# Performance work log

Measured on AMD Instinct MI355X. Metric: run time of the kernel, lower is better.

Reference implementation:

```python
import jax, jax.numpy as jnp
import numpy as np

B, S, DIM = 8, 1, 2048
H = 16
QLR, KVLR = 1536, 512
DN, DR, DV = 128, 64, 128      # qk_nope, qk_rope, v head dims
START = 8191                    # start_pos; end_pos = START + S = 8192
EPS = 1e-6
SCALE = (DN + DR) ** -0.5


def _rms(x, w):
    # F.rms_norm: x / sqrt(mean(x^2)+eps) * w
    return x * w * jax.lax.rsqrt(jnp.mean(jnp.square(x), axis=-1, keepdims=True) + EPS)


def _rope(x, cos, sin):
    # x: [..., r]; consecutive pairs (x0,x1) treated as complex, multiplied by cos+i*sin
    xr, xi = x[..., 0::2], x[..., 1::2]
    out_r = xr * cos - xi * sin
    out_i = xr * sin + xi * cos
    return jnp.stack([out_r, out_i], axis=-1).reshape(x.shape)


def setup_inputs() -> dict:
    key = jax.random.key(0)
    ks = jax.random.split(key, 12)
    # rotary tables for the single decode position
    inv_freq = 1.0 / (10000.0 ** (np.arange(0, DR, 2, dtype=np.float32) / DR))  # [DR/2]
    pos = np.arange(START, START + S, dtype=np.float32)[:, None]                # [S,1]
    ang = pos * inv_freq[None, :]                                               # [S, DR/2]
    return {
        "x": jax.random.normal(ks[0], (B, S, DIM), jnp.float32),
        "start_pos": START,
        "freqs_cos": jnp.asarray(np.cos(ang)),
        "freqs_sin": jnp.asarray(np.sin(ang)),
        "kv_cache_prefix": jax.random.normal(ks[1], (B, START, KVLR), jnp.float32),
        "pe_cache_prefix": jax.random.normal(ks[2], (B, START, DR), jnp.float32),
        "wq_a_w": jax.random.normal(ks[3], (QLR, DIM), jnp.float32) * 0.02,
        "wq_a_b": jnp.zeros((QLR,), jnp.float32),
        "q_norm_w": jnp.ones((QLR,), jnp.float32),
        "wq_b_w": jax.random.normal(ks[4], (H * (DN + DR), QLR), jnp.float32) * 0.02,
        "wq_b_b": jnp.zeros((H * (DN + DR),), jnp.float32),
        "wkv_a_w": jax.random.normal(ks[5], (KVLR + DR, DIM), jnp.float32) * 0.02,
        "wkv_a_b": jnp.zeros((KVLR + DR,), jnp.float32),
        "kv_norm_w": jnp.ones((KVLR,), jnp.float32),
        "wkv_b_w": jax.random.normal(ks[6], (H * (DN + DV), KVLR), jnp.float32) * 0.02,
        "wo_w": jax.random.normal(ks[7], (DIM, H * DV), jnp.float32) * 0.02,
        "wo_b": jnp.zeros((DIM,), jnp.float32),
    }


def reference(x, start_pos, freqs_cos, freqs_sin, kv_cache_prefix, pe_cache_prefix,
              wq_a_w, wq_a_b, q_norm_w, wq_b_w, wq_b_b,
              wkv_a_w, wkv_a_b, kv_norm_w, wkv_b_w, wo_w, wo_b):
    b, s, _ = x.shape
    # low-rank query projection
    q = _rms(x @ wq_a_w.T + wq_a_b, q_norm_w) @ wq_b_w.T + wq_b_b
    q = q.reshape(b, s, H, DN + DR)
    q_nope, q_pe = q[..., :DN], q[..., DN:]
    cos = freqs_cos[None, :, None, :]  # [1,s,1,DR/2]
    sin = freqs_sin[None, :, None, :]
    q_pe = _rope(q_pe, cos, sin)
    # compressed KV + rope key branch
    kvpe = x @ wkv_a_w.T + wkv_a_b               # [b,s,KVLR+DR]
    kv, k_pe = kvpe[..., :KVLR], kvpe[..., KVLR:]
    k_pe = _rope(k_pe[:, :, None, :], cos, sin)[:, :, 0, :]
    # weight absorption: project q_nope into latent space through wkv_b's K-part
    wkv_b = wkv_b_w.reshape(H, DN + DV, KVLR)
    q_abs = jnp.einsum('bshd,hdc->bshc', q_nope, wkv_b[:, :DN])
    # append current step to caches
    kv_cache = jnp.concatenate([kv_cache_prefix, _rms(kv, kv_norm_w)], axis=1)  # [b,t,KVLR]
    pe_cache = jnp.concatenate([pe_cache_prefix, k_pe], axis=1)                 # [b,t,DR]
    # attention in latent space (seqlen=1 decode -> no causal mask needed)
    scores = (jnp.einsum('bshc,btc->bsht', q_abs, kv_cache)
              + jnp.einsum('bshr,btr->bsht', q_pe, pe_cache)) * SCALE
    attn = jax.nn.softmax(scores.astype(jnp.float32), axis=-1).astype(x.dtype)
    out = jnp.einsum('bsht,btc->bshc', attn, kv_cache)
    out = jnp.einsum('bshc,hdc->bshd', out, wkv_b[:, DN:])  # V-part of wkv_b
    return out.reshape(b, s, H * DV) @ wo_w.T + wo_b
```

## Files before the change

kernel.cpp:

```cpp
#include <hip/hip_runtime.h>
#include <math.h>

namespace {
constexpr int B_   = 8;
constexpr int DIM_ = 2048;
constexpr int H_   = 16;
constexpr int QLR_ = 1536;
constexpr int KVLR_= 512;
constexpr int DN_  = 128;
constexpr int DR_  = 64;
constexpr int DV_  = 128;
constexpr int TPRE_= 8191;
constexpr int CE_  = 576;
constexpr int NCH_ = 64;
constexpr int CT_  = 128;
constexpr int TS_  = 16;
constexpr int NS_  = CT_ / TS_;
constexpr int PSTR_= 20;
constexpr float EPS_ = 1e-6f;
constexpr float SCALE_ = 0.07216878364870322f;

constexpr size_t WS_QLAT  = 0;
constexpr size_t WS_KVPE  = WS_QLAT  + (size_t)B_*QLR_;
constexpr size_t WS_PENEW = WS_KVPE  + (size_t)B_*CE_;
constexpr size_t WS_QNOPE = WS_PENEW + (size_t)B_*DR_;
constexpr size_t WS_QT    = WS_QNOPE + (size_t)B_*H_*DN_;
constexpr size_t WS_MLOC  = WS_QT    + (size_t)B_*CE_*H_;
constexpr size_t WS_LLOC  = WS_MLOC  + (size_t)B_*H_*NCH_;
constexpr size_t WS_OUT2  = WS_LLOC  + (size_t)B_*H_*NCH_;
constexpr size_t WS_OPART = WS_OUT2  + (size_t)B_*DIM_;
}

__device__ __forceinline__ void gload16(const float* src, float* ldsDst) {
  __builtin_amdgcn_global_load_lds((const __attribute__((address_space(1))) void*)src,
                                   (__attribute__((address_space(3))) void*)ldsDst,
                                   16, 0, 0);
}

__device__ __forceinline__ float rsum16(float v) {
  int x = __float_as_int(v);
  v += __int_as_float(__builtin_amdgcn_update_dpp(0, x, 0xB1, 0xF, 0xF, true));
  x = __float_as_int(v);
  v += __int_as_float(__builtin_amdgcn_update_dpp(0, x, 0x4E, 0xF, 0xF, true));
  x = __float_as_int(v);
  v += __int_as_float(__builtin_amdgcn_update_dpp(0, x, 0x141, 0xF, 0xF, true));
  x = __float_as_int(v);
  v += __int_as_float(__builtin_amdgcn_update_dpp(0, x, 0x140, 0xF, 0xF, true));
  return v;
}

__device__ __forceinline__ void barrier_lgkm() {
  asm volatile("s_waitcnt lgkmcnt(0)" ::: "memory");
  __builtin_amdgcn_s_barrier();
  __builtin_amdgcn_sched_barrier(0);
}

__global__ __launch_bounds__(256) void mla_k1(const float* __restrict__ x,
                                              const float* __restrict__ wqa,
                                              const float* __restrict__ bqa,
                                              const float* __restrict__ wkva,
                                              const float* __restrict__ bkva,
                                              const float* __restrict__ fcos,
                                              const float* __restrict__ fsin,
                                              float* __restrict__ ws) {
  const int w = threadIdx.x >> 6, l = threadIdx.x & 63;
  const int r0 = (blockIdx.x * 4 + w) * 2;
  const float* W; const float* bias; int rr;
  if (r0 < QLR_) { W = wqa;  bias = bqa;  rr = r0; }
  else           { W = wkva; bias = bkva; rr = r0 - QLR_; }
  const float4* w0p = (const float4*)(W + (size_t)rr * DIM_);
  const float4* w1p = (const float4*)(W + (size_t)(rr + 1) * DIM_);
  const float4* x4  = (const float4*)x;
  float4 wv0[8], wv1[8];
#pragma unroll
  for (int j = 0; j < 8; ++j) { wv0[j] = w0p[l + 64 * j]; wv1[j] = w1p[l + 64 * j]; }
  float acc0[B_], acc1[B_];
#pragma unroll
  for (int b = 0; b < B_; ++b) { acc0[b] = 0.f; acc1[b] = 0.f; }
#pragma unroll
  for (int b = 0; b < B_; ++b) {
#pragma unroll
    for (int j = 0; j < 8; ++j) {
      const float4 xv = x4[b * (DIM_ / 4) + l + 64 * j];
      acc0[b] = fmaf(wv0[j].x, xv.x, fmaf(wv0[j].y, xv.y, fmaf(wv0[j].z, xv.z, fmaf(wv0[j].w, xv.w, acc0[b]))));
      acc1[b] = fmaf(wv1[j].x, xv.x, fmaf(wv1[j].y, xv.y, fmaf(wv1[j].z, xv.z, fmaf(wv1[j].w, xv.w, acc1[b]))));
    }
  }
#pragma unroll
  for (int b = 0; b < B_; ++b)
#pragma unroll
    for (int s = 32; s; s >>= 1) {
      acc0[b] += __shfl_xor(acc0[b], s);
      acc1[b] += __shfl_xor(acc1[b], s);
    }
  if (l == 0) {
    const float b0 = bias[rr], b1 = bias[rr + 1];
    if (r0 < QLR_) {
      float* out = ws + WS_QLAT;
#pragma unroll
      for (int b = 0; b < B_; ++b) {
        out[b * QLR_ + r0]     = acc0[b] + b0;
        out[b * QLR_ + r0 + 1] = acc1[b] + b1;
      }
    } else if (rr < KVLR_) {
      float* out = ws + WS_KVPE;
#pragma unroll
      for (int b = 0; b < B_; ++b) {
        out[b * CE_ + rr]     = acc0[b] + b0;
        out[b * CE_ + rr + 1] = acc1[b] + b1;
      }
    } else {
      const int i = (rr - KVLR_) >> 1;
      const float c = fcos[i], s = fsin[i];
      float* pen = ws + WS_PENEW;
#pragma unroll
      for (int b = 0; b < B_; ++b) {
        const float xr = acc0[b] + b0, xi = acc1[b] + b1;
        pen[b * DR_ + 2 * i]     = xr * c - xi * s;
        pen[b * DR_ + 2 * i + 1] = xr * s + xi * c;
      }
    }
  }
}

__global__ __launch_bounds__(256) void mla_k3(const float* __restrict__ qnw,
                                              const float* __restrict__ wqb,
                                              const float* __restrict__ bqb,
                                              const float* __restrict__ fcos,
                                              const float* __restrict__ fsin,
                                              float* __restrict__ ws) {
  __shared__ float qs_s[B_];
  const int tid = threadIdx.x;
  {
    const int bq = tid >> 5, l32 = tid & 31;
    const float4* ql4 = (const float4*)(ws + WS_QLAT + (size_t)bq * QLR_);
    float ss = 0.f;
#pragma unroll
    for (int j = 0; j < 12; ++j) {
      const float4 v = ql4[l32 + 32 * j];
      ss = fmaf(v.x, v.x, fmaf(v.y, v.y, fmaf(v.z, v.z, fmaf(v.w, v.w, ss))));
    }
#pragma unroll
    for (int d = 16; d; d >>= 1) ss += __shfl_xor(ss, d, 32);
    if (l32 == 0) qs_s[bq] = 1.0f / sqrtf(ss / (float)QLR_ + EPS_);
    __syncthreads();
  }
  const int w = tid >> 6, l = tid & 63;
  const int r0 = blockIdx.x * 8 + w * 2;
  const float4* w0p = (const float4*)(wqb + (size_t)r0 * QLR_);
  const float4* w1p = (const float4*)(wqb + (size_t)(r0 + 1) * QLR_);
  const float4* g4  = (const float4*)qnw;
  const float4* x4  = (const float4*)(ws + WS_QLAT);
  float4 wg0[6], wg1[6];
#pragma unroll
  for (int j = 0; j < 6; ++j) {
    const int c4 = l + 64 * j;
    const float4 a = w0p[c4], bb = w1p[c4], g = g4[c4];
    wg0[j].x = a.x * g.x; wg0[j].y = a.y * g.y; wg0[j].z = a.z * g.z; wg0[j].w = a.w * g.w;
    wg1[j].x = bb.x * g.x; wg1[j].y = bb.y * g.y; wg1[j].z = bb.z * g.z; wg1[j].w = bb.w * g.w;
  }
  float acc0[B_], acc1[B_];
#pragma unroll
  for (int b = 0; b < B_; ++b) { acc0[b] = 0.f; acc1[b] = 0.f; }
#pragma unroll
  for (int b = 0; b < B_; ++b) {
#pragma unroll
    for (int j = 0; j < 6; ++j) {
      const float4 xv = x4[b * (QLR_ / 4) + l + 64 * j];
      acc0[b] = fmaf(wg0[j].x, xv.x, fmaf(wg0[j].y, xv.y, fmaf(wg0[j].z, xv.z, fmaf(wg0[j].w, xv.w, acc0[b]))));
      acc1[b] = fmaf(wg1[j].x, xv.x, fmaf(wg1[j].y, xv.y, fmaf(wg1[j].z, xv.z, fmaf(wg1[j].w, xv.w, acc1[b]))));
    }
  }
#pragma unroll
  for (int b = 0; b < B_; ++b)
#pragma unroll
    for (int s = 32; s; s >>= 1) {
      acc0[b] += __shfl_xor(acc0[b], s);
      acc1[b] += __shfl_xor(acc1[b], s);
    }
  if (l == 0) {
    const int h = r0 / (DN_ + DR_);
    const int j0 = r0 - h * (DN_ + DR_);
    const float b0 = bqb[r0], b1 = bqb[r0 + 1];
    if (j0 < DN_) {
      float* qn = ws + WS_QNOPE;
#pragma unroll
      for (int b = 0; b < B_; ++b) {
        const float sb = qs_s[b];
        qn[(b * H_ + h) * DN_ + j0]     = acc0[b] * sb + b0;
        qn[(b * H_ + h) * DN_ + j0 + 1] = acc1[b] * sb + b1;
      }
    } else {
      const int i = (j0 - DN_) >> 1;
      const float c = fcos[i], s = fsin[i];
      float* qTT = ws + WS_QT;
#pragma unroll
      for (int b = 0; b < B_; ++b) {
        const float sb = qs_s[b];
        const float xr = acc0[b] * sb + b0, xi = acc1[b] * sb + b1;
        qTT[((size_t)(b * H_ + h)) * CE_ + KVLR_ + 2 * i]     = xr * c - xi * s;
        qTT[((size_t)(b * H_ + h)) * CE_ + KVLR_ + 2 * i + 1] = xr * s + xi * c;
      }
    }
  }
}

__global__ __launch_bounds__(256) void mla_k4(const float* __restrict__ wkvb,
                                              float* __restrict__ ws) {
  __shared__ float red[7 * 32 * B_];
  const int h = blockIdx.y;
  const int strip = blockIdx.x;
  const int tid = threadIdx.x;
  const int c = tid & 31, dg = tid >> 5;
  const int cg = strip * 32 + c;
  const float* qn = ws + WS_QNOPE;
  float acc[B_];
#pragma unroll
  for (int b = 0; b < B_; ++b) acc[b] = 0.f;
  const float* wp = wkvb + (size_t)h * 256 * KVLR_ + cg;
#pragma unroll
  for (int dd = 0; dd < 16; ++dd) {
    const int d = dg * 16 + dd;
    const float wv = wp[(size_t)d * KVLR_];
#pragma unroll
    for (int b = 0; b < B_; ++b) acc[b] = fmaf(qn[(b * H_ + h) * DN_ + d], wv, acc[b]);
  }
  if (dg > 0) {
#pragma unroll
    for (int b = 0; b < B_; ++b) red[(((dg - 1) * 32) + c) * B_ + b] = acc[b];
  }
  __syncthreads();
  if (dg == 0) {
    float* qTT = ws + WS_QT;
#pragma unroll
    for (int b = 0; b < B_; ++b) {
      float v = acc[b];
#pragma unroll
      for (int g = 0; g < 7; ++g) v += red[(g * 32 + c) * B_ + b];
      qTT[((size_t)(b * H_ + h)) * CE_ + cg] = v;
    }
  }
}

__global__ __launch_bounds__(512) void mla_k5(const float* __restrict__ kvpre,
                                              const float* __restrict__ pepre,
                                              const float* __restrict__ kvnw,
                                              float* __restrict__ ws) {
  __shared__ float kv_lds[2][TS_ * CE_];
  __shared__ float p_lds[TS_ * PSTR_];
  __shared__ float m_st[H_], l_st[H_], f_st[H_];
  __shared__ float redw[8];
  __shared__ float kvs_s;

  const int b = blockIdx.y, chunk = blockIdx.x;
  const int t0 = chunk * CT_;
  const int tid = threadIdx.x;
  const int w = tid >> 6, l = tid & 63;
  const int cs = l & 15;
  const int hl = l >> 4;
  const int tg = w >> 1;
  const int hg = (w & 1) * 4 + hl;
  const int c4p = tid >> 2, h4p = tid & 3;

  const float* kvraw = ws + WS_KVPE + b * CE_;
  const float* penew = ws + WS_PENEW + b * DR_;

  auto stageKV = [&](float* buf, int s) {
    const int ts0 = t0 + s * TS_;
#pragma unroll
    for (int k = 0; k < 5; ++k) {
      const int i = tid + 512 * k;
      if (i < (TS_ * CE_) / 4) {
        const int tl = i / 144;
        const int c4 = i - tl * 144;
        const int tgl = ts0 + tl;
        const float* src;
        if (tgl < TPRE_) {
          src = (c4 < 128) ? (kvpre + ((size_t)b * TPRE_ + tgl) * KVLR_ + 4 * c4)
                           : (pepre + ((size_t)b * TPRE_ + tgl) * DR_ + 4 * (c4 - 128));
        } else {
          src = (c4 < 128) ? (kvraw + 4 * c4) : (penew + 4 * (c4 - 128));
        }
        gload16(src, buf + (size_t)i * 4);
      }
    }
  };

  stageKV(kv_lds[0], 0);

  {
    const float v = ws[WS_KVPE + b * CE_ + tid];
    float ss = v * v;
#pragma unroll
    for (int d = 32; d; d >>= 1) ss += __shfl_xor(ss, d);
    if (l == 0) redw[w] = ss;
    __syncthreads();
    if (tid == 0) {
      float s = 0.f;
#pragma unroll
      for (int g = 0; g < 8; ++g) s += redw[g];
      kvs_s = 1.0f / sqrtf(s / (float)KVLR_ + EPS_);
    }
  }

  float4 q0v[9], q1v[9];
  {
    const float* qb0 = ws + WS_QT + ((size_t)(b * H_) + 2 * hg) * CE_ + cs * 36;
    const float* qb1 = qb0 + CE_;
#pragma unroll
    for (int j = 0; j < 9; ++j) {
      q0v[j] = *(const float4*)(qb0 + 4 * j);
      q1v[j] = *(const float4*)(qb1 + 4 * j);
    }
  }
  if (tid < H_) { m_st[tid] = -3.4e38f; l_st[tid] = 0.f; }

  float o[4][4];
#pragma unroll
  for (int cc = 0; cc < 4; ++cc)
#pragma unroll
    for (int hh = 0; hh < 4; ++hh) o[cc][hh] = 0.f;

  for (int s = 0; s < NS_; ++s) {
    __syncthreads();
    if (s + 1 < NS_) stageKV(kv_lds[(s + 1) & 1], s + 1);
    float* bufc = kv_lds[s & 1];

    if (chunk == NCH_ - 1 && s == NS_ - 1) {
      float* row = bufc + (TS_ - 1) * CE_;
      row[tid] = row[tid] * kvnw[tid] * kvs_s;
      __syncthreads();
    }

    {
      const float* kb = bufc + (tg * 4) * CE_ + cs * 36;
#pragma unroll
      for (int tt = 0; tt < 4; ++tt) {
        const float* kr = kb + tt * CE_;
        float a0 = 0.f, a1 = 0.f;
#pragma unroll
        for (int j = 0; j < 9; ++j) {
          const float4 k = *(const float4*)(kr + 4 * j);
          const float4 qa = q0v[j], qc = q1v[j];
          a0 = fmaf(k.x, qa.x, fmaf(k.y, qa.y, fmaf(k.z, qa.z, fmaf(k.w, qa.w, a0))));
          a1 = fmaf(k.x, qc.x, fmaf(k.y, qc.y, fmaf(k.z, qc.z, fmaf(k.w, qc.w, a1))));
        }
        a0 = rsum16(a0);
        a1 = rsum16(a1);
        if (cs == 0) {
          float2 v; v.x = a0 * SCALE_; v.y = a1 * SCALE_;
          *(float2*)(p_lds + (tg * 4 + tt) * PSTR_ + 2 * hg) = v;
        }
      }
    }
    barrier_lgkm();

    if (tid < 256) {
      const int h2 = tid >> 4, tl2 = tid & 15;
      const float sv = p_lds[tl2 * PSTR_ + h2];
      float msub = sv;
#pragma unroll
      for (int d = 8; d; d >>= 1) msub = fmaxf(msub, __shfl_xor(msub, d, 16));
      const float mold = m_st[h2];
      const float mnew = fmaxf(mold, msub);
      const float e = __expf(sv - mnew);
      float lsum = e;
#pragma unroll
      for (int d = 8; d; d >>= 1) lsum += __shfl_xor(lsum, d, 16);
      p_lds[tl2 * PSTR_ + h2] = e;
      if (tl2 == 0) {
        const float fac = __expf(mold - mnew);
        f_st[h2] = fac;
        l_st[h2] = l_st[h2] * fac + lsum;
        m_st[h2] = mnew;
      }
    }
    barrier_lgkm();

    {
      const float4 fv = *(const float4*)(f_st + 4 * h4p);
#pragma unroll
      for (int cc = 0; cc < 4; ++cc) {
        o[cc][0] *= fv.x; o[cc][1] *= fv.y; o[cc][2] *= fv.z; o[cc][3] *= fv.w;
      }
#pragma unroll 8
      for (int t = 0; t < TS_; ++t) {
        const float4 kq = *(const float4*)(bufc + t * CE_ + 4 * c4p);
        const float4 pq = *(const float4*)(p_lds + t * PSTR_ + 4 * h4p);
        o[0][0] = fmaf(pq.x, kq.x, o[0][0]); o[0][1] = fmaf(pq.y, kq.x, o[0][1]);
        o[0][2] = fmaf(pq.z, kq.x, o[0][2]); o[0][3] = fmaf(pq.w, kq.x, o[0][3]);
        o[1][0] = fmaf(pq.x, kq.y, o[1][0]); o[1][1] = fmaf(pq.y, kq.y, o[1][1]);
        o[1][2] = fmaf(pq.z, kq.y, o[1][2]); o[1][3] = fmaf(pq.w, kq.y, o[1][3]);
        o[2][0] = fmaf(pq.x, kq.z, o[2][0]); o[2][1] = fmaf(pq.y, kq.z, o[2][1]);
        o[2][2] = fmaf(pq.z, kq.z, o[2][2]); o[2][3] = fmaf(pq.w, kq.z, o[2][3]);
        o[3][0] = fmaf(pq.x, kq.w, o[3][0]); o[3][1] = fmaf(pq.y, kq.w, o[3][1]);
        o[3][2] = fmaf(pq.z, kq.w, o[3][2]); o[3][3] = fmaf(pq.w, kq.w, o[3][3]);
      }
    }
  }

  {
    float* Op = ws + WS_OPART;
#pragma unroll
    for (int hh = 0; hh < 4; ++hh) {
      const int h = 4 * h4p + hh;
      float4 v;
      v.x = o[0][hh]; v.y = o[1][hh]; v.z = o[2][hh]; v.w = o[3][hh];
      *(float4*)(Op + ((size_t)(b * H_ + h) * NCH_ + chunk) * KVLR_ + 4 * c4p) = v;
    }
    if (tid < H_) {
      ws[WS_MLOC + (b * H_ + tid) * NCH_ + chunk] = m_st[tid];
      ws[WS_LLOC + (b * H_ + tid) * NCH_ + chunk] = l_st[tid];
    }
  }
}

__global__ __launch_bounds__(256) void mla_k6(const float* __restrict__ wkvb,
                                              float* __restrict__ ws) {
  const int h = blockIdx.x, b = blockIdx.y;
  __shared__ float wgt[NCH_];
  __shared__ float ao[KVLR_];
  __shared__ float Linv;
  const int tid = threadIdx.x;
  if (tid < NCH_) {
    const float m = ws[WS_MLOC + (b * H_ + h) * NCH_ + tid];
    float M = m;
#pragma unroll
    for (int s = 32; s; s >>= 1) M = fmaxf(M, __shfl_xor(M, s));
    const float wv = __expf(m - M);
    wgt[tid] = wv;
    float lv = ws[WS_LLOC + (b * H_ + h) * NCH_ + tid] * wv;
#pragma unroll
    for (int s = 32; s; s >>= 1) lv += __shfl_xor(lv, s);
    if (tid == 0) Linv = 1.0f / lv;
  }
  __syncthreads();
  const float* Ob = ws + WS_OPART + (size_t)(b * H_ + h) * NCH_ * KVLR_;
  float s0 = 0.f, s1 = 0.f;
#pragma unroll 4
  for (int i = 0; i < NCH_; ++i) {
    const float wv = wgt[i];
    s0 = fmaf(wv, Ob[(size_t)i * KVLR_ + tid], s0);
    s1 = fmaf(wv, Ob[(size_t)i * KVLR_ + tid + 256], s1);
  }
  const float li = Linv;
  ao[tid] = s0 * li;
  ao[tid + 256] = s1 * li;
  __syncthreads();

  const int w6 = tid >> 6, l6 = tid & 63;
  const float4 ax = *(const float4*)(ao + 4 * l6);
  const float4 bx = *(const float4*)(ao + 256 + 4 * l6);
  float* out2 = ws + WS_OUT2 + b * DIM_ + h * DV_;
#pragma unroll 2
  for (int k = 0; k < 32; k += 2) {
    const int v0 = w6 * 32 + k;
    const float4* w20 = (const float4*)(wkvb + ((size_t)h * 256 + DN_ + v0) * KVLR_);
    const float4* w21 = (const float4*)(wkvb + ((size_t)h * 256 + DN_ + v0 + 1) * KVLR_);
    const float4 a0 = w20[l6], c0 = w20[64 + l6];
    const float4 a1 = w21[l6], c1 = w21[64 + l6];
    float t0 = fmaf(a0.x, ax.x, fmaf(a0.y, ax.y, fmaf(a0.z, ax.z, fmaf(a0.w, ax.w,
               fmaf(c0.x, bx.x, fmaf(c0.y, bx.y, fmaf(c0.z, bx.z, c0.w * bx.w)))))));
    float t1 = fmaf(a1.x, ax.x, fmaf(a1.y, ax.y, fmaf(a1.z, ax.z, fmaf(a1.w, ax.w,
               fmaf(c1.x, bx.x, fmaf(c1.y, bx.y, fmaf(c1.z, bx.z, c1.w * bx.w)))))));
#pragma unroll
    for (int d = 32; d; d >>= 1) {
      t0 += __shfl_xor(t0, d);
      t1 += __shfl_xor(t1, d);
    }
    if (l6 == 0) { out2[v0] = t0; out2[v0 + 1] = t1; }
  }
}

__global__ __launch_bounds__(256) void mla_k7(const float* __restrict__ wo,
                                              const float* __restrict__ wob,
                                              const float* __restrict__ ws,
                                              float* __restrict__ out) {
  const int w = threadIdx.x >> 6, l = threadIdx.x & 63;
  const int r0 = (blockIdx.x * 4 + w) * 2;
  const float4* w0p = (const float4*)(wo + (size_t)r0 * DIM_);
  const float4* w1p = (const float4*)(wo + (size_t)(r0 + 1) * DIM_);
  const float4* x4  = (const float4*)(ws + WS_OUT2);
  float4 wv0[8], wv1[8];
#pragma unroll
  for (int j = 0; j < 8; ++j) { wv0[j] = w0p[l + 64 * j]; wv1[j] = w1p[l + 64 * j]; }
  float acc0[B_], acc1[B_];
#pragma unroll
  for (int b = 0; b < B_; ++b) { acc0[b] = 0.f; acc1[b] = 0.f; }
#pragma unroll
  for (int b = 0; b < B_; ++b) {
#pragma unroll
    for (int j = 0; j < 8; ++j) {
      const float4 xv = x4[b * (DIM_ / 4) + l + 64 * j];
      acc0[b] = fmaf(wv0[j].x, xv.x, fmaf(wv0[j].y, xv.y, fmaf(wv0[j].z, xv.z, fmaf(wv0[j].w, xv.w, acc0[b]))));
      acc1[b] = fmaf(wv1[j].x, xv.x, fmaf(wv1[j].y, xv.y, fmaf(wv1[j].z, xv.z, fmaf(wv1[j].w, xv.w, acc1[b]))));
    }
  }
#pragma unroll
  for (int b = 0; b < B_; ++b)
#pragma unroll
    for (int s = 32; s; s >>= 1) {
      acc0[b] += __shfl_xor(acc0[b], s);
      acc1[b] += __shfl_xor(acc1[b], s);
    }
  if (l == 0) {
    const float b0 = wob[r0], b1 = wob[r0 + 1];
#pragma unroll
    for (int b = 0; b < B_; ++b) {
      out[b * DIM_ + r0]     = acc0[b] + b0;
      out[b * DIM_ + r0 + 1] = acc1[b] + b1;
    }
  }
}

extern "C" void kernel_launch(void* const* d_in, const int* in_sizes, int n_in,
                              void* d_out, int out_size, void* d_ws, size_t ws_size,
                              hipStream_t stream) {
  (void)in_sizes; (void)n_in; (void)out_size; (void)ws_size;
  const float* x     = (const float*)d_in[0];
  const float* fcos  = (const float*)d_in[2];
  const float* fsin  = (const float*)d_in[3];
  const float* kvpre = (const float*)d_in[4];
  const float* pepre = (const float*)d_in[5];
  const float* wqa   = (const float*)d_in[6];
  const float* bqa   = (const float*)d_in[7];
  const float* qnw   = (const float*)d_in[8];
  const float* wqb   = (const float*)d_in[9];
  const float* bqb   = (const float*)d_in[10];
  const float* wkva  = (const float*)d_in[11];
  const float* bkva  = (const float*)d_in[12];
  const float* kvnw  = (const float*)d_in[13];
  const float* wkvb  = (const float*)d_in[14];
  const float* wo    = (const float*)d_in[15];
  const float* wob   = (const float*)d_in[16];
  float* ws  = (float*)d_ws;
  float* out = (float*)d_out;

  mla_k1<<<dim3((QLR_ + CE_) / 8), dim3(256), 0, stream>>>(x, wqa, bqa, wkva, bkva, fcos, fsin, ws);
  mla_k3<<<dim3(H_ * (DN_ + DR_) / 8), dim3(256), 0, stream>>>(qnw, wqb, bqb, fcos, fsin, ws);
  mla_k4<<<dim3(16, H_), dim3(256), 0, stream>>>(wkvb, ws);
  mla_k5<<<dim3(NCH_, B_), dim3(512), 0, stream>>>(kvpre, pepre, kvnw, ws);
  mla_k6<<<dim3(H_, B_), dim3(256), 0, stream>>>(wkvb, ws);
  mla_k7<<<dim3(DIM_ / 8), dim3(256), 0, stream>>>(wo, wob, ws, out);
}
```

Before: 354.4 us.

## Fuse pre- and post-attention kernels with software grid barriers; regroup heads in attention

Merges the three pre-attention kernels (x projections, q up-projection, q absorption) into one persistent kernel and the two post-attention kernels (combine plus V projection, output projection) into another, separated by atomic-counter grid barriers whose counters are reset with a memset each call. This targets kernel launch overhead and inter-kernel gaps on a small decode workload. It also changes the attention score loop so each thread handles 4 heads across 2 tokens rather than 2 heads across 4 tokens. The barriers assume all 384 and 256 blocks are co-resident, and they add an extra memset launch.

```diff
diff --git a/kernel.cpp b/kernel.cpp
--- a/kernel.cpp
+++ b/kernel.cpp
@@ -17,13 +17,16 @@
 constexpr int TS_  = 16;
 constexpr int NS_  = CT_ / TS_;
 constexpr int PSTR_= 20;
+constexpr int NPRE_= 384;
+constexpr int NPOST_=256;
 constexpr float EPS_ = 1e-6f;
 constexpr float SCALE_ = 0.07216878364870322f;
 
 constexpr size_t WS_QLAT  = 0;
 constexpr size_t WS_KVPE  = WS_QLAT  + (size_t)B_*QLR_;
 constexpr size_t WS_PENEW = WS_KVPE  + (size_t)B_*CE_;
-constexpr size_t WS_QNOPE = WS_PENEW + (size_t)B_*DR_;
+constexpr size_t WS_BAR   = WS_PENEW + (size_t)B_*DR_;
+constexpr size_t WS_QNOPE = WS_BAR   + 16;
 constexpr size_t WS_QT    = WS_QNOPE + (size_t)B_*H_*DN_;
 constexpr size_t WS_MLOC  = WS_QT    + (size_t)B_*CE_*H_;
 constexpr size_t WS_LLOC  = WS_MLOC  + (size_t)B_*H_*NCH_;
@@ -55,189 +58,199 @@
   __builtin_amdgcn_sched_barrier(0);
 }
 
-__global__ __launch_bounds__(256) void mla_k1(const float* __restrict__ x,
-                                              const float* __restrict__ wqa,
-                                              const float* __restrict__ bqa,
-                                              const float* __restrict__ wkva,
-                                              const float* __restrict__ bkva,
-                                              const float* __restrict__ fcos,
-                                              const float* __restrict__ fsin,
-                                              float* __restrict__ ws) {
-  const int w = threadIdx.x >> 6, l = threadIdx.x & 63;
-  const int r0 = (blockIdx.x * 4 + w) * 2;
-  const float* W; const float* bias; int rr;
-  if (r0 < QLR_) { W = wqa;  bias = bqa;  rr = r0; }
-  else           { W = wkva; bias = bkva; rr = r0 - QLR_; }
-  const float4* w0p = (const float4*)(W + (size_t)rr * DIM_);
-  const float4* w1p = (const float4*)(W + (size_t)(rr + 1) * DIM_);
-  const float4* x4  = (const float4*)x;
-  float4 wv0[8], wv1[8];
-#pragma unroll
-  for (int j = 0; j < 8; ++j) { wv0[j] = w0p[l + 64 * j]; wv1[j] = w1p[l + 64 * j]; }
-  float acc0[B_], acc1[B_];
-#pragma unroll
-  for (int b = 0; b < B_; ++b) { acc0[b] = 0.f; acc1[b] = 0.f; }
-#pragma unroll
-  for (int b = 0; b < B_; ++b) {
-#pragma unroll
-    for (int j = 0; j < 8; ++j) {
-      const float4 xv = x4[b * (DIM_ / 4) + l + 64 * j];
-      acc0[b] = fmaf(wv0[j].x, xv.x, fmaf(wv0[j].y, xv.y, fmaf(wv0[j].z, xv.z, fmaf(wv0[j].w, xv.w, acc0[b]))));
-      acc1[b] = fmaf(wv1[j].x, xv.x, fmaf(wv1[j].y, xv.y, fmaf(wv1[j].z, xv.z, fmaf(wv1[j].w, xv.w, acc1[b]))));
-    }
-  }
-#pragma unroll
-  for (int b = 0; b < B_; ++b)
-#pragma unroll
-    for (int s = 32; s; s >>= 1) {
-      acc0[b] += __shfl_xor(acc0[b], s);
-      acc1[b] += __shfl_xor(acc1[b], s);
-    }
-  if (l == 0) {
-    const float b0 = bias[rr], b1 = bias[rr + 1];
-    if (r0 < QLR_) {
-      float* out = ws + WS_QLAT;
+__device__ __forceinline__ void gridbar(unsigned* bar, unsigned target) {
+  __syncthreads();
+  if (threadIdx.x == 0) {
+    __threadfence();
+    atomicAdd(bar, 1u);
+    int guard = 0;
+    while (__hip_atomic_load(bar, __ATOMIC_ACQUIRE, __HIP_MEMORY_SCOPE_AGENT) < target) {
+      __builtin_amdgcn_s_sleep(2);
+      if (++guard > (1 << 28)) break;
+    }
+  }
+  __syncthreads();
+}
+
+__global__ __launch_bounds__(256) void mla_pre(
+    const float* __restrict__ x, const float* __restrict__ fcos, const float* __restrict__ fsin,
+    const float* __restrict__ wqa, const float* __restrict__ bqa,
+    const float* __restrict__ qnw, const float* __restrict__ wqb, const float* __restrict__ bqb,
+    const float* __restrict__ wkva, const float* __restrict__ bkva,
+    const float* __restrict__ wkvb, float* __restrict__ ws) {
+  __shared__ float red[7 * 32 * B_];
+  __shared__ float qs_s[B_];
+  unsigned* bar = (unsigned*)(ws + WS_BAR);
+  const int bid = blockIdx.x;
+  const int tid = threadIdx.x;
+  const int w = tid >> 6, l = tid & 63;
+
+  if (bid < 264) {
+    const int r0 = (bid * 4 + w) * 2;
+    const float* W; const float* bias; int rr;
+    if (r0 < QLR_) { W = wqa;  bias = bqa;  rr = r0; }
+    else           { W = wkva; bias = bkva; rr = r0 - QLR_; }
+    const float4* w0p = (const float4*)(W + (size_t)rr * DIM_);
+    const float4* w1p = (const float4*)(W + (size_t)(rr + 1) * DIM_);
+    const float4* x4  = (const float4*)x;
+    float4 wv0[8], wv1[8];
+#pragma unroll
+    for (int j = 0; j < 8; ++j) { wv0[j] = w0p[l + 64 * j]; wv1[j] = w1p[l + 64 * j]; }
+    float acc0[B_], acc1[B_];
+#pragma unroll
+    for (int b = 0; b < B_; ++b) { acc0[b] = 0.f; acc1[b] = 0.f; }
+#pragma unroll
+    for (int b = 0; b < B_; ++b) {
+#pragma unroll
+      for (int j = 0; j < 8; ++j) {
+        const float4 xv = x4[b * (DIM_ / 4) + l + 64 * j];
+        acc0[b] = fmaf(wv0[j].x, xv.x, fmaf(wv0[j].y, xv.y, fmaf(wv0[j].z, xv.z, fmaf(wv0[j].w, xv.w, acc0[b]))));
+        acc1[b] = fmaf(wv1[j].x, xv.x, fmaf(wv1[j].y, xv.y, fmaf(wv1[j].z, xv.z, fmaf(wv1[j].w, xv.w, acc1[b]))));
+      }
+    }
+#pragma unroll
+    for (int b = 0; b < B_; ++b)
+#pragma unroll
+      for (int s = 32; s; s >>= 1) {
+        acc0[b] += __shfl_xor(acc0[b], s);
+        acc1[b] += __shfl_xor(acc1[b], s);
+      }
+    if (l == 0) {
+      const float b0 = bias[rr], b1 = bias[rr + 1];
+      if (r0 < QLR_) {
+        float* outp = ws + WS_QLAT;
+#pragma unroll
+        for (int b = 0; b < B_; ++b) {
+          outp[b * QLR_ + r0]     = acc0[b] + b0;
+          outp[b * QLR_ + r0 + 1] = acc1[b] + b1;
+        }
+      } else if (rr < KVLR_) {
+        float* outp = ws + WS_KVPE;
+#pragma unroll
+        for (int b = 0; b < B_; ++b) {
+          outp[b * CE_ + rr]     = acc0[b] + b0;
+          outp[b * CE_ + rr + 1] = acc1[b] + b1;
+        }
+      } else {
+        const int i = (rr - KVLR_) >> 1;
+        const float c = fcos[i], s = fsin[i];
+        float* pen = ws + WS_PENEW;
+#pragma unroll
+        for (int b = 0; b < B_; ++b) {
+          const float xr = acc0[b] + b0, xi = acc1[b] + b1;
+          pen[b * DR_ + 2 * i]     = xr * c - xi * s;
+          pen[b * DR_ + 2 * i + 1] = xr * s + xi * c;
+        }
+      }
+    }
+  }
+  gridbar(bar, NPRE_);
+
+  {
+    {
+      const int bq = tid >> 5, l32 = tid & 31;
+      const float4* ql4 = (const float4*)(ws + WS_QLAT + (size_t)bq * QLR_);
+      float ss = 0.f;
+#pragma unroll
+      for (int j = 0; j < 12; ++j) {
+        const float4 v = ql4[l32 + 32 * j];
+        ss = fmaf(v.x, v.x, fmaf(v.y, v.y, fmaf(v.z, v.z, fmaf(v.w, v.w, ss))));
+      }
+#pragma unroll
+      for (int d = 16; d; d >>= 1) ss += __shfl_xor(ss, d, 32);
+      if (l32 == 0) qs_s[bq] = 1.0f / sqrtf(ss / (float)QLR_ + EPS_);
+      __syncthreads();
+    }
+    const int r0 = bid * 8 + w * 2;
+    const float4* w0p = (const float4*)(wqb + (size_t)r0 * QLR_);
+    const float4* w1p = (const float4*)(wqb + (size_t)(r0 + 1) * QLR_);
+    const float4* g4  = (const float4*)qnw;
+    const float4* x4  = (const float4*)(ws + WS_QLAT);
+    float4 wg0[6], wg1[6];
+#pragma unroll
+    for (int j = 0; j < 6; ++j) {
+      const int c4 = l + 64 * j;
+      const float4 a = w0p[c4], bb = w1p[c4], g = g4[c4];
+      wg0[j].x = a.x * g.x; wg0[j].y = a.y * g.y; wg0[j].z = a.z * g.z; wg0[j].w = a.w * g.w;
+      wg1[j].x = bb.x * g.x; wg1[j].y = bb.y * g.y; wg1[j].z = bb.z * g.z; wg1[j].w = bb.w * g.w;
+    }
+    float acc0[B_], acc1[B_];
+#pragma unroll
+    for (int b = 0; b < B_; ++b) { acc0[b] = 0.f; acc1[b] = 0.f; }
+#pragma unroll
+    for (int b = 0; b < B_; ++b) {
+#pragma unroll
+      for (int j = 0; j < 6; ++j) {
+        const float4 xv = x4[b * (QLR_ / 4) + l + 64 * j];
+        acc0[b] = fmaf(wg0[j].x, xv.x, fmaf(wg0[j].y, xv.y, fmaf(wg0[j].z, xv.z, fmaf(wg0[j].w, xv.w, acc0[b]))));
+        acc1[b] = fmaf(wg1[j].x, xv.x, fmaf(wg1[j].y, xv.y, fmaf(wg1[j].z, xv.z, fmaf(wg1[j].w, xv.w, acc1[b]))));
+      }
+    }
+#pragma unroll
+    for (int b = 0; b < B_; ++b)
+#pragma unroll
+      for (int s = 32; s; s >>= 1) {
+        acc0[b] += __shfl_xor(acc0[b], s);
+        acc1[b] += __shfl_xor(acc1[b], s);
+      }
+    if (l == 0) {
+      const int h = r0 / (DN_ + DR_);
+      const int j0 = r0 - h * (DN_ + DR_);
+      const float b0 = bqb[r0], b1 = bqb[r0 + 1];
+      if (j0 < DN_) {
+        float* qn = ws + WS_QNOPE;
+#pragma unroll
+        for (int b = 0; b < B_; ++b) {
+          const float sb = qs_s[b];
+          qn[(b * H_ + h) * DN_ + j0]     = acc0[b] * sb + b0;
+          qn[(b * H_ + h) * DN_ + j0 + 1] = acc1[b] * sb + b1;
+        }
+      } else {
+        const int i = (j0 - DN_) >> 1;
+        const float c = fcos[i], s = fsin[i];
+        float* qTT = ws + WS_QT;
+#pragma unroll
+        for (int b = 0; b < B_; ++b) {
+          const float sb = qs_s[b];
+          const float xr = acc0[b] * sb + b0, xi = acc1[b] * sb + b1;
+          qTT[((size_t)(b * H_ + h)) * CE_ + KVLR_ + 2 * i]     = xr * c - xi * s;
+          qTT[((size_t)(b * H_ + h)) * CE_ + KVLR_ + 2 * i + 1] = xr * s + xi * c;
+        }
+      }
+    }
+  }
+  gridbar(bar, 2 * NPRE_);
+
+  if (bid < 256) {
+    const int h = bid >> 4, strip = bid & 15;
+    const int c = tid & 31, dg = tid >> 5;
+    const int cg = strip * 32 + c;
+    const float* qn = ws + WS_QNOPE;
+    float acc[B_];
+#pragma unroll
+    for (int b = 0; b < B_; ++b) acc[b] = 0.f;
+    const float* wp = wkvb + (size_t)h * 256 * KVLR_ + cg;
+#pragma unroll
+    for (int dd = 0; dd < 16; ++dd) {
+      const int d = dg * 16 + dd;
+      const float wv = wp[(size_t)d * KVLR_];
+#pragma unroll
+      for (int b = 0; b < B_; ++b) acc[b] = fmaf(qn[(b * H_ + h) * DN_ + d], wv, acc[b]);
+    }
+    if (dg > 0) {
+#pragma unroll
+      for (int b = 0; b < B_; ++b) red[(((dg - 1) * 32) + c) * B_ + b] = acc[b];
+    }
+    __syncthreads();
+    if (dg == 0) {
+      float* qTT = ws + WS_QT;
 #pragma unroll
       for (int b = 0; b < B_; ++b) {
-        out[b * QLR_ + r0]     = acc0[b] + b0;
-        out[b * QLR_ + r0 + 1] = acc1[b] + b1;
-      }
-    } else if (rr < KVLR_) {
-      float* out = ws + WS_KVPE;
-#pragma unroll
-      for (int b = 0; b < B_; ++b) {
-        out[b * CE_ + rr]     = acc0[b] + b0;
-        out[b * CE_ + rr + 1] = acc1[b] + b1;
-      }
-    } else {
-      const int i = (rr - KVLR_) >> 1;
-      const float c = fcos[i], s = fsin[i];
-      float* pen = ws + WS_PENEW;
-#pragma unroll
-      for (int b = 0; b < B_; ++b) {
-        const float xr = acc0[b] + b0, xi = acc1[b] + b1;
-        pen[b * DR_ + 2 * i]     = xr * c - xi * s;
-        pen[b * DR_ + 2 * i + 1] = xr * s + xi * c;
-      }
-    }
-  }
-}
-
-__global__ __launch_bounds__(256) void mla_k3(const float* __restrict__ qnw,
-                                              const float* __restrict__ wqb,
-                                              const float* __restrict__ bqb,
-                                              const float* __restrict__ fcos,
-                                              const float* __restrict__ fsin,
-                                              float* __restrict__ ws) {
-  __shared__ float qs_s[B_];
-  const int tid = threadIdx.x;
-  {
-    const int bq = tid >> 5, l32 = tid & 31;
-    const float4* ql4 = (const float4*)(ws + WS_QLAT + (size_t)bq * QLR_);
-    float ss = 0.f;
-#pragma unroll
-    for (int j = 0; j < 12; ++j) {
-      const float4 v = ql4[l32 + 32 * j];
-      ss = fmaf(v.x, v.x, fmaf(v.y, v.y, fmaf(v.z, v.z, fmaf(v.w, v.w, ss))));
-    }
-#pragma unroll
-    for (int d = 16; d; d >>= 1) ss += __shfl_xor(ss, d, 32);
-    if (l32 == 0) qs_s[bq] = 1.0f / sqrtf(ss / (float)QLR_ + EPS_);
-    __syncthreads();
-  }
-  const int w = tid >> 6, l = tid & 63;
-  const int r0 = blockIdx.x * 8 + w * 2;
-  const float4* w0p = (const float4*)(wqb + (size_t)r0 * QLR_);
-  const float4* w1p = (const float4*)(wqb + (size_t)(r0 + 1) * QLR_);
-  const float4* g4  = (const float4*)qnw;
-  const float4* x4  = (const float4*)(ws + WS_QLAT);
-  float4 wg0[6], wg1[6];
-#pragma unroll
-  for (int j = 0; j < 6; ++j) {
-    const int c4 = l + 64 * j;
-    const float4 a = w0p[c4], bb = w1p[c4], g = g4[c4];
-    wg0[j].x = a.x * g.x; wg0[j].y = a.y * g.y; wg0[j].z = a.z * g.z; wg0[j].w = a.w * g.w;
-    wg1[j].x = bb.x * g.x; wg1[j].y = bb.y * g.y; wg1[j].z = bb.z * g.z; wg1[j].w = bb.w * g.w;
-  }
-  float acc0[B_], acc1[B_];
-#pragma unroll
-  for (int b = 0; b < B_; ++b) { acc0[b] = 0.f; acc1[b] = 0.f; }
-#pragma unroll
-  for (int b = 0; b < B_; ++b) {
-#pragma unroll
-    for (int j = 0; j < 6; ++j) {
-      const float4 xv = x4[b * (QLR_ / 4) + l + 64 * j];
-      acc0[b] = fmaf(wg0[j].x, xv.x, fmaf(wg0[j].y, xv.y, fmaf(wg0[j].z, xv.z, fmaf(wg0[j].w, xv.w, acc0[b]))));
-      acc1[b] = fmaf(wg1[j].x, xv.x, fmaf(wg1[j].y, xv.y, fmaf(wg1[j].z, xv.z, fmaf(wg1[j].w, xv.w, acc1[b]))));
-    }
-  }
-#pragma unroll
-  for (int b = 0; b < B_; ++b)
-#pragma unroll
-    for (int s = 32; s; s >>= 1) {
-      acc0[b] += __shfl_xor(acc0[b], s);
-      acc1[b] += __shfl_xor(acc1[b], s);
-    }
-  if (l == 0) {
-    const int h = r0 / (DN_ + DR_);
-    const int j0 = r0 - h * (DN_ + DR_);
-    const float b0 = bqb[r0], b1 = bqb[r0 + 1];
-    if (j0 < DN_) {
-      float* qn = ws + WS_QNOPE;
-#pragma unroll
-      for (int b = 0; b < B_; ++b) {
-        const float sb = qs_s[b];
-        qn[(b * H_ + h) * DN_ + j0]     = acc0[b] * sb + b0;
-        qn[(b * H_ + h) * DN_ + j0 + 1] = acc1[b] * sb + b1;
-      }
-    } else {
-      const int i = (j0 - DN_) >> 1;
-      const float c = fcos[i], s = fsin[i];
-      float* qTT = ws + WS_QT;
-#pragma unroll
-      for (int b = 0; b < B_; ++b) {
-        const float sb = qs_s[b];
-        const float xr = acc0[b] * sb + b0, xi = acc1[b] * sb + b1;
-        qTT[((size_t)(b * H_ + h)) * CE_ + KVLR_ + 2 * i]     = xr * c - xi * s;
-        qTT[((size_t)(b * H_ + h)) * CE_ + KVLR_ + 2 * i + 1] = xr * s + xi * c;
-      }
-    }
-  }
-}
-
-__global__ __launch_bounds__(256) void mla_k4(const float* __restrict__ wkvb,
-                                              float* __restrict__ ws) {
-  __shared__ float red[7 * 32 * B_];
-  const int h = blockIdx.y;
-  const int strip = blockIdx.x;
-  const int tid = threadIdx.x;
-  const int c = tid & 31, dg = tid >> 5;
-  const int cg = strip * 32 + c;
-  const float* qn = ws + WS_QNOPE;
-  float acc[B_];
-#pragma unroll
-  for (int b = 0; b < B_; ++b) acc[b] = 0.f;
-  const float* wp = wkvb + (size_t)h * 256 * KVLR_ + cg;
-#pragma unroll
-  for (int dd = 0; dd < 16; ++dd) {
-    const int d = dg * 16 + dd;
-    const float wv = wp[(size_t)d * KVLR_];
-#pragma unroll
-    for (int b = 0; b < B_; ++b) acc[b] = fmaf(qn[(b * H_ + h) * DN_ + d], wv, acc[b]);
-  }
-  if (dg > 0) {
-#pragma unroll
-    for (int b = 0; b < B_; ++b) red[(((dg - 1) * 32) + c) * B_ + b] = acc[b];
-  }
-  __syncthreads();
-  if (dg == 0) {
-    float* qTT = ws + WS_QT;
-#pragma unroll
-    for (int b = 0; b < B_; ++b) {
-      float v = acc[b];
-#pragma unroll
-      for (int g = 0; g < 7; ++g) v += red[(g * 32 + c) * B_ + b];
-      qTT[((size_t)(b * H_ + h)) * CE_ + cg] = v;
+        float v = acc[b];
+#pragma unroll
+        for (int g = 0; g < 7; ++g) v += red[(g * 32 + c) * B_ + b];
+        qTT[((size_t)(b * H_ + h)) * CE_ + cg] = v;
+      }
     }
   }
 }
@@ -257,9 +270,7 @@
   const int tid = threadIdx.x;
   const int w = tid >> 6, l = tid & 63;
   const int cs = l & 15;
-  const int hl = l >> 4;
-  const int tg = w >> 1;
-  const int hg = (w & 1) * 4 + hl;
+  const int hg = (l >> 4) & 3;
   const int c4p = tid >> 2, h4p = tid & 3;
 
   const float* kvraw = ws + WS_KVPE + b * CE_;
@@ -303,14 +314,15 @@
     }
   }
 
-  float4 q0v[9], q1v[9];
+  float4 qv0[9], qv1[9], qv2[9], qv3[9];
   {
-    const float* qb0 = ws + WS_QT + ((size_t)(b * H_) + 2 * hg) * CE_ + cs * 36;
-    const float* qb1 = qb0 + CE_;
+    const float* qb = ws + WS_QT + ((size_t)(b * H_) + 4 * hg) * CE_ + cs * 36;
 #pragma unroll
     for (int j = 0; j < 9; ++j) {
-      q0v[j] = *(const float4*)(qb0 + 4 * j);
-      q1v[j] = *(const float4*)(qb1 + 4 * j);
+      qv0[j] = *(const float4*)(qb + 0 * CE_ + 4 * j);
+      qv1[j] = *(const float4*)(qb + 1 * CE_ + 4 * j);
+      qv2[j] = *(const float4*)(qb + 2 * CE_ + 4 * j);
+      qv3[j] = *(const float4*)(qb + 3 * CE_ + 4 * j);
     }
   }
   if (tid < H_) { m_st[tid] = -3.4e38f; l_st[tid] = 0.f; }
@@ -333,24 +345,32 @@
     }
 
     {
-      const float* kb = bufc + (tg * 4) * CE_ + cs * 36;
-#pragma unroll
-      for (int tt = 0; tt < 4; ++tt) {
-        const float* kr = kb + tt * CE_;
-        float a0 = 0.f, a1 = 0.f;
-#pragma unroll
-        for (int j = 0; j < 9; ++j) {
-          const float4 k = *(const float4*)(kr + 4 * j);
-          const float4 qa = q0v[j], qc = q1v[j];
-          a0 = fmaf(k.x, qa.x, fmaf(k.y, qa.y, fmaf(k.z, qa.z, fmaf(k.w, qa.w, a0))));
-          a1 = fmaf(k.x, qc.x, fmaf(k.y, qc.y, fmaf(k.z, qc.z, fmaf(k.w, qc.w, a1))));
-        }
-        a0 = rsum16(a0);
-        a1 = rsum16(a1);
-        if (cs == 0) {
-          float2 v; v.x = a0 * SCALE_; v.y = a1 * SCALE_;
-          *(float2*)(p_lds + (tg * 4 + tt) * PSTR_ + 2 * hg) = v;
-        }
+      const float* kr0 = bufc + (w * 2) * CE_ + cs * 36;
+      const float* kr1 = kr0 + CE_;
+      float a00 = 0.f, a01 = 0.f, a02 = 0.f, a03 = 0.f;
+      float a10 = 0.f, a11 = 0.f, a12 = 0.f, a13 = 0.f;
+#pragma unroll
+      for (int j = 0; j < 9; ++j) {
+        const float4 k0 = *(const float4*)(kr0 + 4 * j);
+        const float4 k1 = *(const float4*)(kr1 + 4 * j);
+        const float4 q0 = qv0[j], q1 = qv1[j], q2 = qv2[j], q3 = qv3[j];
+        a00 = fmaf(k0.x, q0.x, fmaf(k0.y, q0.y, fmaf(k0.z, q0.z, fmaf(k0.w, q0.w, a00))));
+        a01 = fmaf(k0.x, q1.x, fmaf(k0.y, q1.y, fmaf(k0.z, q1.z, fmaf(k0.w, q1.w, a01))));
+        a02 = fmaf(k0.x, q2.x, fmaf(k0.y, q2.y, fmaf(k0.z, q2.z, fmaf(k0.w, q2.w, a02))));
+        a03 = fmaf(k0.x, q3.x, fmaf(k0.y, q3.y, fmaf(k0.z, q3.z, fmaf(k0.w, q3.w, a03))));
+        a10 = fmaf(k1.x, q0.x, fmaf(k1.y, q0.y, fmaf(k1.z, q0.z, fmaf(k1.w, q0.w, a10))));
+        a11 = fmaf(k1.x, q1.x, fmaf(k1.y, q1.y, fmaf(k1.z, q1.z, fmaf(k1.w, q1.w, a11))));
+        a12 = fmaf(k1.x, q2.x, fmaf(k1.y, q2.y, fmaf(k1.z, q2.z, fmaf(k1.w, q2.w, a12))));
+        a13 = fmaf(k1.x, q3.x, fmaf(k1.y, q3.y, fmaf(k1.z, q3.z, fmaf(k1.w, q3.w, a13))));
+      }
+      a00 = rsum16(a00); a01 = rsum16(a01); a02 = rsum16(a02); a03 = rsum16(a03);
+      a10 = rsum16(a10); a11 = rsum16(a11); a12 = rsum16(a12); a13 = rsum16(a13);
+      if (cs == 0) {
+        float4 v0, v1;
+        v0.x = a00 * SCALE_; v0.y = a01 * SCALE_; v0.z = a02 * SCALE_; v0.w = a03 * SCALE_;
+        v1.x = a10 * SCALE_; v1.y = a11 * SCALE_; v1.z = a12 * SCALE_; v1.w = a13 * SCALE_;
+        *(float4*)(p_lds + (w * 2) * PSTR_ + 4 * hg)     = v0;
+        *(float4*)(p_lds + (w * 2 + 1) * PSTR_ + 4 * hg) = v1;
       }
     }
     barrier_lgkm();
@@ -415,100 +435,105 @@
   }
 }
 
-__global__ __launch_bounds__(256) void mla_k6(const float* __restrict__ wkvb,
-                                              float* __restrict__ ws) {
-  const int h = blockIdx.x, b = blockIdx.y;
+__global__ __launch_bounds__(256) void mla_post(const float* __restrict__ wkvb,
+                                                const float* __restrict__ wo,
+                                                const float* __restrict__ wob,
+                                                float* __restrict__ ws,
+                                                float* __restrict__ out) {
   __shared__ float wgt[NCH_];
   __shared__ float ao[KVLR_];
   __shared__ float Linv;
+  unsigned* bar = (unsigned*)(ws + WS_BAR) + 1;
+  const int bid = blockIdx.x;
   const int tid = threadIdx.x;
-  if (tid < NCH_) {
-    const float m = ws[WS_MLOC + (b * H_ + h) * NCH_ + tid];
-    float M = m;
-#pragma unroll
-    for (int s = 32; s; s >>= 1) M = fmaxf(M, __shfl_xor(M, s));
-    const float wv = __expf(m - M);
-    wgt[tid] = wv;
-    float lv = ws[WS_LLOC + (b * H_ + h) * NCH_ + tid] * wv;
-#pragma unroll
-    for (int s = 32; s; s >>= 1) lv += __shfl_xor(lv, s);
-    if (tid == 0) Linv = 1.0f / lv;
-  }
-  __syncthreads();
-  const float* Ob = ws + WS_OPART + (size_t)(b * H_ + h) * NCH_ * KVLR_;
-  float s0 = 0.f, s1 = 0.f;
+  const int w = tid >> 6, l = tid & 63;
+
+  if (bid < H_ * B_) {
+    const int h = bid & 15, b = bid >> 4;
+    if (tid < NCH_) {
+      const float m = ws[WS_MLOC + (b * H_ + h) * NCH_ + tid];
+      float M = m;
+#pragma unroll
+      for (int s = 32; s; s >>= 1) M = fmaxf(M, __shfl_xor(M, s));
+      const float wv = __expf(m - M);
+      wgt[tid] = wv;
+      float lv = ws[WS_LLOC + (b * H_ + h) * NCH_ + tid] * wv;
+#pragma unroll
+      for (int s = 32; s; s >>= 1) lv += __shfl_xor(lv, s);
+      if (tid == 0) Linv = 1.0f / lv;
+    }
+    __syncthreads();
+    const float* Ob = ws + WS_OPART + (size_t)(b * H_ + h) * NCH_ * KVLR_;
+    float s0 = 0.f, s1 = 0.f;
 #pragma unroll 4
-  for (int i = 0; i < NCH_; ++i) {
-    const float wv = wgt[i];
-    s0 = fmaf(wv, Ob[(size_t)i * KVLR_ + tid], s0);
-    s1 = fmaf(wv, Ob[(size_t)i * KVLR_ + tid + 256], s1);
-  }
-  const float li = Linv;
-  ao[tid] = s0 * li;
-  ao[tid + 256] = s1 * li;
-  __syncthreads();
-
-  const int w6 = tid >> 6, l6 = tid & 63;
-  const float4 ax = *(const float4*)(ao + 4 * l6);
-  const float4 bx = *(const float4*)(ao + 256 + 4 * l6);
-  float* out2 = ws + WS_OUT2 + b * DIM_ + h * DV_;
+    for (int i = 0; i < NCH_; ++i) {
+      const float wv = wgt[i];
+      s0 = fmaf(wv, Ob[(size_t)i * KVLR_ + tid], s0);
+      s1 = fmaf(wv, Ob[(size_t)i * KVLR_ + tid + 256], s1);
+    }
+    const float li = Linv;
+    ao[tid] = s0 * li;
+    ao[tid + 256] = s1 * li;
+    __syncthreads();
+
+    const float4 ax = *(const float4*)(ao + 4 * l);
+    const float4 bx = *(const float4*)(ao + 256 + 4 * l);
+    float* out2 = ws + WS_OUT2 + b * DIM_ + h * DV_;
 #pragma unroll 2
-  for (int k = 0; k < 32; k += 2) {
-    const int v0 = w6 * 32 + k;
-    const float4* w20 = (const float4*)(wkvb + ((size_t)h * 256 + DN_ + v0) * KVLR_);
-    const float4* w21 = (const float4*)(wkvb + ((size_t)h * 256 + DN_ + v0 + 1) * KVLR_);
-    const float4 a0 = w20[l6], c0 = w20[64 + l6];
-    const float4 a1 = w21[l6], c1 = w21[64 + l6];
-    float t0 = fmaf(a0.x, ax.x, fmaf(a0.y, ax.y, fmaf(a0.z, ax.z, fmaf(a0.w, ax.w,
-               fmaf(c0.x, bx.x, fmaf(c0.y, bx.y, fmaf(c0.z, bx.z, c0.w * bx.w)))))));
-    float t1 = fmaf(a1.x, ax.x, fmaf(a1.y, ax.y, fmaf(a1.z, ax.z, fmaf(a1.w, ax.w,
-               fmaf(c1.x, bx.x, fmaf(c1.y, bx.y, fmaf(c1.z, bx.z, c1.w * bx.w)))))));
-#pragma unroll
-    for (int d = 32; d; d >>= 1) {
-      t0 += __shfl_xor(t0, d);
-      t1 += __shfl_xor(t1, d);
-    }
-    if (l6 == 0) { out2[v0] = t0; out2[v0 + 1] = t1; }
-  }
-}
-
-__global__ __launch_bounds__(256) void mla_k7(const float* __restrict__ wo,
-                                              const float* __restrict__ wob,
-                                              const float* __restrict__ ws,
-                                              float* __restrict__ out) {
-  const int w = threadIdx.x >> 6, l = threadIdx.x & 63;
-  const int r0 = (blockIdx.x * 4 + w) * 2;
-  const float4* w0p = (const float4*)(wo + (size_t)r0 * DIM_);
-  const float4* w1p = (const float4*)(wo + (size_t)(r0 + 1) * DIM_);
-  const float4* x4  = (const float4*)(ws + WS_OUT2);
-  float4 wv0[8], wv1[8];
-#pragma unroll
-  for (int j = 0; j < 8; ++j) { wv0[j] = w0p[l + 64 * j]; wv1[j] = w1p[l + 64 * j]; }
-  float acc0[B_], acc1[B_];
-#pragma unroll
-  for (int b = 0; b < B_; ++b) { acc0[b] = 0.f; acc1[b] = 0.f; }
-#pragma unroll
-  for (int b = 0; b < B_; ++b) {
-#pragma unroll
-    for (int j = 0; j < 8; ++j) {
-      const float4 xv = x4[b * (DIM_ / 4) + l + 64 * j];
-      acc0[b] = fmaf(wv0[j].x, xv.x, fmaf(wv0[j].y, xv.y, fmaf(wv0[j].z, xv.z, fmaf(wv0[j].w, xv.w, acc0[b]))));
-      acc1[b] = fmaf(wv1[j].x, xv.x, fmaf(wv1[j].y, xv.y, fmaf(wv1[j].z, xv.z, fmaf(wv1[j].w, xv.w, acc1[b]))));
-    }
-  }
-#pragma unroll
-  for (int b = 0; b < B_; ++b)
-#pragma unroll
-    for (int s = 32; s; s >>= 1) {
-      acc0[b] += __shfl_xor(acc0[b], s);
-      acc1[b] += __shfl_xor(acc1[b], s);
-    }
-  if (l == 0) {
-    const float b0 = wob[r0], b1 = wob[r0 + 1];
+    for (int k = 0; k < 32; k += 2) {
+      const int v0 = w * 32 + k;
+      const float4* w20 = (const float4*)(wkvb + ((size_t)h * 256 + DN_ + v0) * KVLR_);
+      const float4* w21 = (const float4*)(wkvb + ((size_t)h * 256 + DN_ + v0 + 1) * KVLR_);
+      const float4 a0 = w20[l], c0 = w20[64 + l];
+      const float4 a1 = w21[l], c1 = w21[64 + l];
+      float t0 = fmaf(a0.x, ax.x, fmaf(a0.y, ax.y, fmaf(a0.z, ax.z, fmaf(a0.w, ax.w,
+                 fmaf(c0.x, bx.x, fmaf(c0.y, bx.y, fmaf(c0.z, bx.z, c0.w * bx.w)))))));
+      float t1 = fmaf(a1.x, ax.x, fmaf(a1.y, ax.y, fmaf(a1.z, ax.z, fmaf(a1.w, ax.w,
+                 fmaf(c1.x, bx.x, fmaf(c1.y, bx.y, fmaf(c1.z, bx.z, c1.w * bx.w)))))));
+#pragma unroll
+      for (int d = 32; d; d >>= 1) {
+        t0 += __shfl_xor(t0, d);
+        t1 += __shfl_xor(t1, d);
+      }
+      if (l == 0) { out2[v0] = t0; out2[v0 + 1] = t1; }
+    }
+  }
+  gridbar(bar, NPOST_);
+
+  {
+    const int r0 = (bid * 4 + w) * 2;
+    const float4* w0p = (const float4*)(wo + (size_t)r0 * DIM_);
+    const float4* w1p = (const float4*)(wo + (size_t)(r0 + 1) * DIM_);
+    const float4* x4  = (const float4*)(ws + WS_OUT2);
+    float4 wv0[8], wv1[8];
+#pragma unroll
+    for (int j = 0; j < 8; ++j) { wv0[j] = w0p[l + 64 * j]; wv1[j] = w1p[l + 64 * j]; }
+    float acc0[B_], acc1[B_];
+#pragma unroll
+    for (int b = 0; b < B_; ++b) { acc0[b] = 0.f; acc1[b] = 0.f; }
 #pragma unroll
     for (int b = 0; b < B_; ++b) {
-      out[b * DIM_ + r0]     = acc0[b] + b0;
-      out[b * DIM_ + r0 + 1] = acc1[b] + b1;
+#pragma unroll
+      for (int j = 0; j < 8; ++j) {
+        const float4 xv = x4[b * (DIM_ / 4) + l + 64 * j];
+        acc0[b] = fmaf(wv0[j].x, xv.x, fmaf(wv0[j].y, xv.y, fmaf(wv0[j].z, xv.z, fmaf(wv0[j].w, xv.w, acc0[b]))));
+        acc1[b] = fmaf(wv1[j].x, xv.x, fmaf(wv1[j].y, xv.y, fmaf(wv1[j].z, xv.z, fmaf(wv1[j].w, xv.w, acc1[b]))));
+      }
+    }
+#pragma unroll
+    for (int b = 0; b < B_; ++b)
+#pragma unroll
+      for (int s = 32; s; s >>= 1) {
+        acc0[b] += __shfl_xor(acc0[b], s);
+        acc1[b] += __shfl_xor(acc1[b], s);
+      }
+    if (l == 0) {
+      const float b0 = wob[r0], b1 = wob[r0 + 1];
+#pragma unroll
+      for (int b = 0; b < B_; ++b) {
+        out[b * DIM_ + r0]     = acc0[b] + b0;
+        out[b * DIM_ + r0 + 1] = acc1[b] + b1;
+      }
     }
   }
 }
@@ -536,10 +561,9 @@
   float* ws  = (float*)d_ws;
   float* out = (float*)d_out;
 
-  mla_k1<<<dim3((QLR_ + CE_) / 8), dim3(256), 0, stream>>>(x, wqa, bqa, wkva, bkva, fcos, fsin, ws);
-  mla_k3<<<dim3(H_ * (DN_ + DR_) / 8), dim3(256), 0, stream>>>(qnw, wqb, bqb, fcos, fsin, ws);
-  mla_k4<<<dim3(16, H_), dim3(256), 0, stream>>>(wkvb, ws);
+  hipMemsetAsync((char*)d_ws + WS_BAR * sizeof(float), 0, 16, stream);
+  mla_pre<<<dim3(NPRE_), dim3(256), 0, stream>>>(x, fcos, fsin, wqa, bqa, qnw, wqb, bqb,
+                                                 wkva, bkva, wkvb, ws);
   mla_k5<<<dim3(NCH_, B_), dim3(512), 0, stream>>>(kvpre, pepre, kvnw, ws);
-  mla_k6<<<dim3(H_, B_), dim3(256), 0, stream>>>(wkvb, ws);
-  mla_k7<<<dim3(DIM_ / 8), dim3(256), 0, stream>>>(wo, wob, ws, out);
-}
+  mla_post<<<dim3(NPOST_), dim3(256), 0, stream>>>(wkvb, wo, wob, ws, out);
+}
```

New measurement: 489.0 us. 1.38x slower.
